# Kernel tuning notes

Hardware: AMD Instinct MI355X
Metric: run time of the kernel (lower is better)

Reference implementation:

```python
import jax, jax.numpy as jnp
import numpy as np

N = 50000; F = 128; H = 128; E = 800000; G = 512; C = 1000; CE = 64; L = 128
EPS = 1e-5

def gcn_conv(x, src, dst, W, b, num_nodes):
    # PyG GCNConv: add self loops, sym-normalize, aggregate at dst
    loop = jnp.arange(num_nodes)
    s = jnp.concatenate([src, loop])
    d = jnp.concatenate([dst, loop])
    deg = jax.ops.segment_sum(jnp.ones_like(d, dtype=x.dtype), d, num_segments=num_nodes)
    dinv = jnp.where(deg > 0, jax.lax.rsqrt(deg), 0.0)
    norm = dinv[s] * dinv[d]                      # [E+N]
    h = x @ W                                     # [N,H]
    msg = h[s] * norm[:, None]                    # gather + scale
    return jax.ops.segment_sum(msg, d, num_segments=num_nodes) + b

def layer_norm(x, w, b):
    mu = jnp.mean(x, axis=-1, keepdims=True)
    var = jnp.var(x, axis=-1, keepdims=True)
    return (x - mu) * jax.lax.rsqrt(var + EPS) * w + b

def setup_inputs() -> dict:
    key = jax.random.key(0)
    ks = jax.random.split(key, 16)
    x = jax.random.normal(ks[0], (N, F), dtype=jnp.float32)
    edge_index = jax.random.randint(ks[1], (2, E), 0, N)
    batch = jnp.sort(jax.random.randint(ks[2], (N,), 0, G))
    cell_lines = jax.random.randint(ks[3], (G,), 0, C)
    def kai(k, shape):
        fan_in = shape[0]
        bound = np.sqrt(6.0 / fan_in)
        return jax.random.uniform(k, shape, jnp.float32, -bound, bound)
    return {
        'x': x, 'edge_index': edge_index, 'batch': batch, 'cell_lines': cell_lines,
        'W1': kai(ks[4], (F, H)), 'b1': jnp.zeros((H,), jnp.float32),
        'W2': kai(ks[5], (H, H)), 'b2': jnp.zeros((H,), jnp.float32),
        'emb': jax.random.normal(ks[6], (C, CE), dtype=jnp.float32),
        'Wc': kai(ks[7], (H + CE, H)), 'bc': jnp.zeros((H,), jnp.float32),
        'lnc_w': jnp.ones((H,), jnp.float32), 'lnc_b': jnp.zeros((H,), jnp.float32),
        'Wf1': kai(ks[8], (H, H)), 'bf1': jnp.zeros((H,), jnp.float32),
        'ln1_w': jnp.ones((H,), jnp.float32), 'ln1_b': jnp.zeros((H,), jnp.float32),
        'Wf2': kai(ks[9], (H, L)), 'bf2': jnp.zeros((L,), jnp.float32),
    }

def reference(x, edge_index, batch, cell_lines, W1, b1, W2, b2, emb, Wc, bc,
              lnc_w, lnc_b, Wf1, bf1, ln1_w, ln1_b, Wf2, bf2):
    src, dst = edge_index[0], edge_index[1]
    h = jax.nn.relu(gcn_conv(x, src, dst, W1, b1, N))
    h = jax.nn.relu(gcn_conv(h, src, dst, W2, b2, N))
    g = jax.ops.segment_sum(h, batch, num_segments=G)          # global_add_pool [G,H]
    ce = emb[cell_lines]                                       # [G,CE]
    comb = jnp.concatenate([g, ce], axis=1)
    comb = jax.nn.relu(layer_norm(comb @ Wc + bc, lnc_w, lnc_b))
    out = jax.nn.relu(comb @ Wf1 + bf1)                        # dropout = identity (eval)
    out = layer_norm(out, ln1_w, ln1_b)
    return out @ Wf2 + bf2
```

## Files before the change

### kernel.cpp

```cpp
#include <hip/hip_runtime.h>

#define N_NODES 50000
#define NFEAT 128
#define NEDGE 800000
#define NGRAPH 512
#define NCE 64
#define EPS 1e-5f
#define NBUCK 196
#define EPB 4096
#define BCAP 6144

typedef short s8v __attribute__((ext_vector_type(8)));
typedef float f4v __attribute__((ext_vector_type(4)));

static __device__ __forceinline__ unsigned short f2bf(float f) {
    unsigned int u = __float_as_uint(f);
    unsigned int r = u + 0x7fffu + ((u >> 16) & 1u);
    return (unsigned short)(r >> 16);
}
static __device__ __forceinline__ float bf_lo(unsigned int packed) {
    return __uint_as_float(packed << 16);
}
static __device__ __forceinline__ float bf_hi(unsigned int packed) {
    return __uint_as_float(packed & 0xffff0000u);
}
static __device__ __forceinline__ float bf_us(unsigned short us) {
    return __uint_as_float(((unsigned int)us) << 16);
}

__global__ __launch_bounds__(256) void wcast_kernel(
    const float* __restrict__ W1, const float* __restrict__ W2,
    unsigned short* __restrict__ WT1, unsigned short* __restrict__ WT2,
    int* __restrict__ bucketCursor)
{
    if (blockIdx.x == 0 && blockIdx.y == 0 && threadIdx.x < NBUCK)
        bucketCursor[threadIdx.x] = 0;
    const float* W = blockIdx.y ? W2 : W1;
    unsigned short* WT = blockIdx.y ? WT2 : WT1;
    int idx = blockIdx.x * 256 + threadIdx.x;
    int k = idx >> 7, n = idx & 127;
    WT[n * 128 + k] = f2bf(W[idx]);
}

__global__ __launch_bounds__(256) void bucket_scatter_kernel(
    const int* __restrict__ ei, int* __restrict__ bucketCursor,
    unsigned int* __restrict__ recbuf, int E)
{
    __shared__ int hist[NBUCK];
    __shared__ int lbase[NBUCK];
    __shared__ int gbase[NBUCK];
    __shared__ int cur[NBUCK];
    __shared__ int scanbuf[256];
    __shared__ unsigned int staging[EPB];
    int tid = threadIdx.x;
    if (tid < NBUCK) { hist[tid] = 0; cur[tid] = 0; }
    __syncthreads();

    unsigned int rec[EPB / 256];
    int e0 = blockIdx.x * EPB + tid;
#pragma unroll
    for (int i = 0; i < EPB / 256; ++i) {
        int e = e0 + i * 256;
        if (e < E) {
            unsigned int sv = (unsigned)ei[e];
            unsigned int dv = (unsigned)ei[E + e];
            rec[i] = sv | (dv << 16);
            atomicAdd(&hist[dv >> 8], 1);
        } else {
            rec[i] = 0xffffffffu;
        }
    }
    __syncthreads();
    int v = (tid < NBUCK) ? hist[tid] : 0;
    scanbuf[tid] = v; __syncthreads();
    for (int off = 1; off < 256; off <<= 1) {
        int t = (tid >= off) ? scanbuf[tid - off] : 0;
        __syncthreads();
        scanbuf[tid] += t;
        __syncthreads();
    }
    if (tid < NBUCK) lbase[tid] = scanbuf[tid] - v;
    int total = scanbuf[255];
    if (tid < NBUCK) gbase[tid] = (v > 0) ? atomicAdd(&bucketCursor[tid], v) : 0;
    __syncthreads();
#pragma unroll
    for (int i = 0; i < EPB / 256; ++i) {
        if (rec[i] != 0xffffffffu) {
            int b = rec[i] >> 24;
            int loc = atomicAdd(&cur[b], 1);
            staging[lbase[b] + loc] = rec[i];
        }
    }
    __syncthreads();
    for (int s = tid; s < total; s += 256) {
        unsigned int r = staging[s];
        int b = r >> 24;
        int pos = gbase[b] + (s - lbase[b]);
        if (pos < BCAP) recbuf[(size_t)b * BCAP + pos] = r;
    }
}

__global__ __launch_bounds__(256) void bucket_csr_kernel(
    const unsigned int* __restrict__ recbuf, const int* __restrict__ bucketCursor,
    int* __restrict__ rowbeg, unsigned short* __restrict__ deg,
    float* __restrict__ dinv, unsigned short* __restrict__ colidx)
{
    __shared__ int cnt[256];
    __shared__ int cur[256];
    __shared__ int scanbuf[256];
    __shared__ unsigned short stage[BCAP];
    int b = blockIdx.x, tid = threadIdx.x;
    int base = b * BCAP;
    int len = bucketCursor[b]; if (len > BCAP) len = BCAP;
    cnt[tid] = 0;
    __syncthreads();
    for (int s = tid; s < len; s += 256) {
        unsigned int r = recbuf[base + s];
        atomicAdd(&cnt[(r >> 16) & 255], 1);
    }
    __syncthreads();
    int v = cnt[tid];
    scanbuf[tid] = v; __syncthreads();
    for (int off = 1; off < 256; off <<= 1) {
        int t = (tid >= off) ? scanbuf[tid - off] : 0;
        __syncthreads();
        scanbuf[tid] += t;
        __syncthreads();
    }
    int excl = scanbuf[tid] - v;
    int node = b * 256 + tid;
    if (node < N_NODES) {
        rowbeg[node] = base + excl;
        deg[node] = (unsigned short)v;
        dinv[node] = rsqrtf((float)v + 1.0f);
    }
    cur[tid] = excl;
    __syncthreads();
    for (int s = tid; s < len; s += 256) {
        unsigned int r = recbuf[base + s];
        int pos = atomicAdd(&cur[(r >> 16) & 255], 1);
        stage[pos] = (unsigned short)(r & 0xffffu);
    }
    __syncthreads();
    for (int s = tid; s < len; s += 256) colidx[base + s] = stage[s];
}

template<bool FP32IN>
__global__ __launch_bounds__(256) void gemm_mfma_kernel(
    const void* __restrict__ Ain, const unsigned short* __restrict__ WTg,
    const float* __restrict__ dinv, unsigned short* __restrict__ HS, int nrows)
{
    __shared__ unsigned short as[128 * 128];
    __shared__ unsigned short wt[128 * 128];
    const int tid = threadIdx.x;
    const int row0 = blockIdx.x * 128;

    {
        const uint4* src = reinterpret_cast<const uint4*>(WTg);
        uint4* dst = reinterpret_cast<uint4*>(wt);
#pragma unroll
        for (int i = 0; i < 8; ++i) dst[tid + i * 256] = src[tid + i * 256];
    }
    if (FP32IN) {
        const float* X = (const float*)Ain;
#pragma unroll
        for (int i = 0; i < 16; ++i) {
            int f = tid + i * 256;
            int r = f >> 5, c4 = f & 31;
            int rr = row0 + r; if (rr >= nrows) rr = nrows - 1;
            float4 v = *reinterpret_cast<const float4*>(&X[rr * 128 + c4 * 4]);
            ushort4 o;
            o.x = f2bf(v.x); o.y = f2bf(v.y); o.z = f2bf(v.z); o.w = f2bf(v.w);
            *reinterpret_cast<ushort4*>(&as[r * 128 + c4 * 4]) = o;
        }
    } else {
        const unsigned short* X = (const unsigned short*)Ain;
#pragma unroll
        for (int i = 0; i < 8; ++i) {
            int f = tid + i * 256;
            int r = f >> 4, c8 = f & 15;
            int rr = row0 + r; if (rr >= nrows) rr = nrows - 1;
            *reinterpret_cast<uint4*>(&as[r * 128 + c8 * 8]) =
                *reinterpret_cast<const uint4*>(&X[rr * 128 + c8 * 8]);
        }
    }
    __syncthreads();

    const int w = tid >> 6;
    const int lane = tid & 63;
    const int quad = lane >> 4;
    const int col0 = lane & 15;

    s8v afr[2][4];
#pragma unroll
    for (int rt = 0; rt < 2; ++rt)
#pragma unroll
        for (int kt = 0; kt < 4; ++kt)
            afr[rt][kt] = *reinterpret_cast<const s8v*>(
                &as[(w * 32 + rt * 16 + col0) * 128 + kt * 32 + quad * 8]);

    f4v acc[2][8];
#pragma unroll
    for (int rt = 0; rt < 2; ++rt)
#pragma unroll
        for (int nt = 0; nt < 8; ++nt)
            acc[rt][nt] = (f4v){0.f, 0.f, 0.f, 0.f};

#pragma unroll
    for (int nt = 0; nt < 8; ++nt) {
        s8v bfr[4];
#pragma unroll
        for (int kt = 0; kt < 4; ++kt)
            bfr[kt] = *reinterpret_cast<const s8v*>(
                &wt[(nt * 16 + col0) * 128 + kt * 32 + quad * 8]);
#pragma unroll
        for (int rt = 0; rt < 2; ++rt)
#pragma unroll
            for (int kt = 0; kt < 4; ++kt)
                acc[rt][nt] = __builtin_amdgcn_mfma_f32_16x16x32_bf16(
                    afr[rt][kt], bfr[kt], acc[rt][nt], 0, 0, 0);
    }

    float dv[2][4];
#pragma unroll
    for (int rt = 0; rt < 2; ++rt)
#pragma unroll
        for (int reg = 0; reg < 4; ++reg) {
            int r = row0 + w * 32 + rt * 16 + quad * 4 + reg;
            dv[rt][reg] = (r < nrows) ? dinv[r] : 0.f;
        }

#pragma unroll
    for (int rt = 0; rt < 2; ++rt)
#pragma unroll
        for (int nt = 0; nt < 8; ++nt)
#pragma unroll
            for (int reg = 0; reg < 4; ++reg) {
                int rl = w * 32 + rt * 16 + quad * 4 + reg;
                as[rl * 128 + nt * 16 + col0] = f2bf(acc[rt][nt][reg] * dv[rt][reg]);
            }
    __syncthreads();
#pragma unroll
    for (int i = 0; i < 8; ++i) {
        int f = tid + i * 256;
        int r = f >> 4, c8 = f & 15;
        if (row0 + r < nrows)
            *reinterpret_cast<uint4*>(&HS[(size_t)(row0 + r) * 128 + c8 * 8]) =
                *reinterpret_cast<const uint4*>(&as[r * 128 + c8 * 8]);
    }
}

__global__ __launch_bounds__(256) void aggregate_kernel(
    const uint2* __restrict__ H2,
    const int* __restrict__ rowbeg, const unsigned short* __restrict__ deg,
    const unsigned short* __restrict__ colidx,
    const float* __restrict__ dinv, const float* __restrict__ bias,
    uint2* __restrict__ OUT, int n)
{
    int wid = (blockIdx.x * blockDim.x + threadIdx.x) >> 6;
    int lane = threadIdx.x & 63;
    if (wid >= n) return;
    const int half = lane >> 5;
    const int sub = lane & 31;
    int beg = rowbeg[wid];
    int cnt = (int)deg[wid] + 1;
    float s0 = 0.f, s1 = 0.f, s2 = 0.f, s3 = 0.f;
    float r0 = 0.f, r1 = 0.f, r2 = 0.f, r3 = 0.f;
    for (int base = 0; base < cnt; base += 64) {
        int m = cnt - base; if (m > 64) m = 64;
        int p = base + lane;
        int idx = 0;
        if (lane < m) idx = (p == 0) ? wid : (int)colidx[beg + p - 1];
        int j = 0;
        for (; j + 16 <= m; j += 16) {
            uint2 t[8];
#pragma unroll
            for (int q = 0; q < 8; ++q) {
                int u = __shfl(idx, j + q * 2 + half);
                t[q] = H2[(size_t)u * 32 + sub];
            }
#pragma unroll
            for (int q = 0; q < 8; q += 2) {
                s0 += bf_lo(t[q].x); s1 += bf_hi(t[q].x);
                s2 += bf_lo(t[q].y); s3 += bf_hi(t[q].y);
                r0 += bf_lo(t[q + 1].x); r1 += bf_hi(t[q + 1].x);
                r2 += bf_lo(t[q + 1].y); r3 += bf_hi(t[q + 1].y);
            }
        }
        for (; j + 4 <= m; j += 4) {
            int ua = __shfl(idx, j + half);
            int ub = __shfl(idx, j + 2 + half);
            uint2 ta = H2[(size_t)ua * 32 + sub];
            uint2 tb = H2[(size_t)ub * 32 + sub];
            s0 += bf_lo(ta.x); s1 += bf_hi(ta.x);
            s2 += bf_lo(ta.y); s3 += bf_hi(ta.y);
            r0 += bf_lo(tb.x); r1 += bf_hi(tb.x);
            r2 += bf_lo(tb.y); r3 += bf_hi(tb.y);
        }
        if (j + 2 <= m) {
            int u = __shfl(idx, j + half);
            uint2 t = H2[(size_t)u * 32 + sub];
            s0 += bf_lo(t.x); s1 += bf_hi(t.x);
            s2 += bf_lo(t.y); s3 += bf_hi(t.y);
            j += 2;
        }
        if (j < m) {
            int u = __shfl(idx, j);
            uint2 t; t.x = 0u; t.y = 0u;
            if (half == 0) t = H2[(size_t)u * 32 + sub];
            s0 += bf_lo(t.x); s1 += bf_hi(t.x);
            s2 += bf_lo(t.y); s3 += bf_hi(t.y);
        }
    }
    s0 += r0; s1 += r1; s2 += r2; s3 += r3;
    s0 += __shfl_xor(s0, 32);
    s1 += __shfl_xor(s1, 32);
    s2 += __shfl_xor(s2, 32);
    s3 += __shfl_xor(s3, 32);
    if (half == 0) {
        float sc = dinv[wid];
        float4 bv = *reinterpret_cast<const float4*>(&bias[sub * 4]);
        float o0 = fmaxf(fmaf(s0, sc, bv.x), 0.f);
        float o1 = fmaxf(fmaf(s1, sc, bv.y), 0.f);
        float o2 = fmaxf(fmaf(s2, sc, bv.z), 0.f);
        float o3 = fmaxf(fmaf(s3, sc, bv.w), 0.f);
        uint2 o;
        o.x = (unsigned int)f2bf(o0) | ((unsigned int)f2bf(o1) << 16);
        o.y = (unsigned int)f2bf(o2) | ((unsigned int)f2bf(o3) << 16);
        OUT[(size_t)wid * 32 + sub] = o;
    }
}

__global__ __launch_bounds__(256) void tail_kernel(
    const unsigned short* __restrict__ h2b, const int* __restrict__ batch,
    const int* __restrict__ cell, const float* __restrict__ emb,
    const float* __restrict__ Wc, const float* __restrict__ bc,
    const float* __restrict__ lncw, const float* __restrict__ lncb,
    const float* __restrict__ Wf1, const float* __restrict__ bf1,
    const float* __restrict__ ln1w, const float* __restrict__ ln1b,
    const float* __restrict__ Wf2, const float* __restrict__ bf2,
    float* __restrict__ out)
{
    __shared__ __align__(16) float comb[192];
    __shared__ __align__(16) float part[8][132];
    __shared__ float red[4];
    __shared__ __align__(16) float vec[128];
    const int gi = blockIdx.x;
    const int tid = threadIdx.x;
    const int cg = tid & 31;
    const int ks = tid >> 5;

    int lo = 0, hi = N_NODES;
    while (lo < hi) { int mid = (lo + hi) >> 1; if (batch[mid] < gi) lo = mid + 1; else hi = mid; }
    int lo2 = lo, hi2 = N_NODES;
    while (lo2 < hi2) { int mid = (lo2 + hi2) >> 1; if (batch[mid] < gi + 1) lo2 = mid + 1; else hi2 = mid; }

    {
        int half = tid >> 7;
        int j = tid & 127;
        float acc = 0.f;
        for (int v = lo + half; v < lo2; v += 2)
            acc += bf_us(h2b[(size_t)v * 128 + j]);
        part[half][j] = acc;
    }
    __syncthreads();
    if (tid < 128) comb[tid] = part[0][tid] + part[1][tid];
    else if (tid < 192) comb[tid] = emb[cell[gi] * 64 + (tid - 128)];
    __syncthreads();

    {
        float c[24];
#pragma unroll
        for (int i = 0; i < 6; ++i) {
            float4 t = *reinterpret_cast<const float4*>(&comb[ks * 24 + i * 4]);
            c[i * 4 + 0] = t.x; c[i * 4 + 1] = t.y; c[i * 4 + 2] = t.z; c[i * 4 + 3] = t.w;
        }
        float a0 = 0.f, a1 = 0.f, a2 = 0.f, a3 = 0.f;
#pragma unroll
        for (int i = 0; i < 24; ++i) {
            const float4 w = *reinterpret_cast<const float4*>(&Wc[(ks * 24 + i) * 128 + cg * 4]);
            a0 = fmaf(c[i], w.x, a0);
            a1 = fmaf(c[i], w.y, a1);
            a2 = fmaf(c[i], w.z, a2);
            a3 = fmaf(c[i], w.w, a3);
        }
        float4 o; o.x = a0; o.y = a1; o.z = a2; o.w = a3;
        *reinterpret_cast<float4*>(&part[ks][cg * 4]) = o;
    }
    __syncthreads();
    {
        float y = 0.f;
        if (tid < 128) {
            y = bc[tid];
#pragma unroll
            for (int s = 0; s < 8; ++s) y += part[s][tid];
        }
        float s1 = (tid < 128) ? y : 0.f;
        float s2 = (tid < 128) ? y * y : 0.f;
        if (tid < 128) {
#pragma unroll
            for (int off = 32; off > 0; off >>= 1) {
                s1 += __shfl_down(s1, off);
                s2 += __shfl_down(s2, off);
            }
            if ((tid & 63) == 0) { red[(tid >> 6) * 2] = s1; red[(tid >> 6) * 2 + 1] = s2; }
        }
        __syncthreads();
        float mu = (red[0] + red[2]) * (1.f / 128.f);
        float ms = (red[1] + red[3]) * (1.f / 128.f);
        float var = ms - mu * mu;
        if (tid < 128) {
            float yv = (y - mu) * rsqrtf(var + EPS) * lncw[tid] + lncb[tid];
            vec[tid] = fmaxf(yv, 0.f);
        }
    }
    __syncthreads();

    {
        float c[16];
#pragma unroll
        for (int i = 0; i < 4; ++i) {
            float4 t = *reinterpret_cast<const float4*>(&vec[ks * 16 + i * 4]);
            c[i * 4 + 0] = t.x; c[i * 4 + 1] = t.y; c[i * 4 + 2] = t.z; c[i * 4 + 3] = t.w;
        }
        float a0 = 0.f, a1 = 0.f, a2 = 0.f, a3 = 0.f;
#pragma unroll
        for (int i = 0; i < 16; ++i) {
            const float4 w = *reinterpret_cast<const float4*>(&Wf1[(ks * 16 + i) * 128 + cg * 4]);
            a0 = fmaf(c[i], w.x, a0);
            a1 = fmaf(c[i], w.y, a1);
            a2 = fmaf(c[i], w.z, a2);
            a3 = fmaf(c[i], w.w, a3);
        }
        float4 o; o.x = a0; o.y = a1; o.z = a2; o.w = a3;
        *reinterpret_cast<float4*>(&part[ks][cg * 4]) = o;
    }
    __syncthreads();
    {
        float y = 0.f;
        if (tid < 128) {
            y = bf1[tid];
#pragma unroll
            for (int s = 0; s < 8; ++s) y += part[s][tid];
            y = fmaxf(y, 0.f);
        }
        float s1 = (tid < 128) ? y : 0.f;
        float s2 = (tid < 128) ? y * y : 0.f;
        if (tid < 128) {
#pragma unroll
            for (int off = 32; off > 0; off >>= 1) {
                s1 += __shfl_down(s1, off);
                s2 += __shfl_down(s2, off);
            }
            if ((tid & 63) == 0) { red[(tid >> 6) * 2] = s1; red[(tid >> 6) * 2 + 1] = s2; }
        }
        __syncthreads();
        float mu = (red[0] + red[2]) * (1.f / 128.f);
        float ms = (red[1] + red[3]) * (1.f / 128.f);
        float var = ms - mu * mu;
        if (tid < 128)
            vec[tid] = (y - mu) * rsqrtf(var + EPS) * ln1w[tid] + ln1b[tid];
    }
    __syncthreads();

    {
        float c[16];
#pragma unroll
        for (int i = 0; i < 4; ++i) {
            float4 t = *reinterpret_cast<const float4*>(&vec[ks * 16 + i * 4]);
            c[i * 4 + 0] = t.x; c[i * 4 + 1] = t.y; c[i * 4 + 2] = t.z; c[i * 4 + 3] = t.w;
        }
        float a0 = 0.f, a1 = 0.f, a2 = 0.f, a3 = 0.f;
#pragma unroll
        for (int i = 0; i < 16; ++i) {
            const float4 w = *reinterpret_cast<const float4*>(&Wf2[(ks * 16 + i) * 128 + cg * 4]);
            a0 = fmaf(c[i], w.x, a0);
            a1 = fmaf(c[i], w.y, a1);
            a2 = fmaf(c[i], w.z, a2);
            a3 = fmaf(c[i], w.w, a3);
        }
        float4 o; o.x = a0; o.y = a1; o.z = a2; o.w = a3;
        *reinterpret_cast<float4*>(&part[ks][cg * 4]) = o;
    }
    __syncthreads();
    if (tid < 128) {
        float y = bf2[tid];
#pragma unroll
        for (int s = 0; s < 8; ++s) y += part[s][tid];
        out[gi * 128 + tid] = y;
    }
}

extern "C" void kernel_launch(void* const* d_in, const int* in_sizes, int n_in,
                              void* d_out, int out_size, void* d_ws, size_t ws_size,
                              hipStream_t stream) {
    const float* x    = (const float*)d_in[0];
    const int*   ei   = (const int*)d_in[1];
    const int*   batch= (const int*)d_in[2];
    const int*   cell = (const int*)d_in[3];
    const float* W1   = (const float*)d_in[4];
    const float* b1   = (const float*)d_in[5];
    const float* W2   = (const float*)d_in[6];
    const float* b2   = (const float*)d_in[7];
    const float* emb  = (const float*)d_in[8];
    const float* Wc   = (const float*)d_in[9];
    const float* bc   = (const float*)d_in[10];
    const float* lncw = (const float*)d_in[11];
    const float* lncb = (const float*)d_in[12];
    const float* Wf1  = (const float*)d_in[13];
    const float* bf1  = (const float*)d_in[14];
    const float* ln1w = (const float*)d_in[15];
    const float* ln1b = (const float*)d_in[16];
    const float* Wf2  = (const float*)d_in[17];
    const float* bf2  = (const float*)d_in[18];
    float* out = (float*)d_out;

    char* ws = (char*)d_ws;
    size_t off = 0;
    auto alloc = [&](size_t bytes) { char* p = ws + off; off = (off + bytes + 255) & ~size_t(255); return p; };
    float*          dinv        = (float*)alloc(N_NODES * 4);
    int*            rowbeg      = (int*)  alloc(N_NODES * 4);
    unsigned short* deg         = (unsigned short*)alloc(N_NODES * 2);
    unsigned short* colidx      = (unsigned short*)alloc((size_t)NBUCK * BCAP * 2);
    int*            bucketCursor= (int*)  alloc(NBUCK * 4);
    unsigned int*   recbuf      = (unsigned int*)alloc((size_t)NBUCK * BCAP * 4);
    unsigned short* wt1         = (unsigned short*)alloc(128 * 128 * 2);
    unsigned short* wt2         = (unsigned short*)alloc(128 * 128 * 2);
    unsigned short* hs          = (unsigned short*)alloc((size_t)N_NODES * 128 * 2);
    unsigned short* h1          = (unsigned short*)alloc((size_t)N_NODES * 128 * 2);
    unsigned short* h2b         = (unsigned short*)alloc((size_t)N_NODES * 128 * 2);

    const int nbEdge = (NEDGE + EPB - 1) / EPB;
    const int nbGemm = (N_NODES + 127) / 128;
    const int nbAgg  = (N_NODES + 3) / 4;

    wcast_kernel<<<dim3(64, 2), 256, 0, stream>>>(W1, W2, wt1, wt2, bucketCursor);

    bucket_scatter_kernel<<<nbEdge, 256, 0, stream>>>(ei, bucketCursor, recbuf, NEDGE);
    bucket_csr_kernel<<<NBUCK, 256, 0, stream>>>(recbuf, bucketCursor, rowbeg, deg, dinv, colidx);

    gemm_mfma_kernel<true><<<nbGemm, 256, 0, stream>>>(x, wt1, dinv, hs, N_NODES);
    aggregate_kernel<<<nbAgg, 256, 0, stream>>>((const uint2*)hs, rowbeg, deg, colidx,
                                                dinv, b1, (uint2*)h1, N_NODES);
    gemm_mfma_kernel<false><<<nbGemm, 256, 0, stream>>>(h1, wt2, dinv, hs, N_NODES);
    aggregate_kernel<<<nbAgg, 256, 0, stream>>>((const uint2*)hs, rowbeg, deg, colidx,
                                                dinv, b2, (uint2*)h2b, N_NODES);
    tail_kernel<<<NGRAPH, 256, 0, stream>>>(h2b, batch, cell, emb, Wc, bc, lncw, lncb,
                                            Wf1, bf1, ln1w, ln1b, Wf2, bf2, out);
}
```

Baseline: 243.2 us.

## Use per-block fixed bucket slots, fuse weight cast, widen aggregate loads

Bucket scatter now writes each block's records into a fixed per-(bucket, block) slot of 64 entries and records per-slot counts. This removes the global atomic cursor and its zeroing, which lets the weight-cast work fold into the same launch and drops one kernel. The CSR kernel walks those slots using the counts. The aggregation kernel switches from 8-byte to 16-byte row loads, with four rows per wavefront step instead of two. The trade-offs are a much larger, sparsely filled record buffer that the CSR kernel must scan, and edges beyond 64 per slot are silently dropped.

```diff
diff --git a/kernel.cpp b/kernel.cpp
--- a/kernel.cpp
+++ b/kernel.cpp
@@ -8,6 +8,8 @@
 #define EPS 1e-5f
 #define NBUCK 196
 #define EPB 4096
+#define NSCAT 196
+#define CPB 64
 #define BCAP 6144
 
 typedef short s8v __attribute__((ext_vector_type(8)));
@@ -28,36 +30,33 @@
     return __uint_as_float(((unsigned int)us) << 16);
 }
 
-__global__ __launch_bounds__(256) void wcast_kernel(
+__global__ __launch_bounds__(256) void scatter_wcast_kernel(
+    const int* __restrict__ ei,
     const float* __restrict__ W1, const float* __restrict__ W2,
     unsigned short* __restrict__ WT1, unsigned short* __restrict__ WT2,
-    int* __restrict__ bucketCursor)
+    unsigned int* __restrict__ recbuf, unsigned short* __restrict__ cnts, int E)
 {
-    if (blockIdx.x == 0 && blockIdx.y == 0 && threadIdx.x < NBUCK)
-        bucketCursor[threadIdx.x] = 0;
-    const float* W = blockIdx.y ? W2 : W1;
-    unsigned short* WT = blockIdx.y ? WT2 : WT1;
-    int idx = blockIdx.x * 256 + threadIdx.x;
-    int k = idx >> 7, n = idx & 127;
-    WT[n * 128 + k] = f2bf(W[idx]);
-}
-
-__global__ __launch_bounds__(256) void bucket_scatter_kernel(
-    const int* __restrict__ ei, int* __restrict__ bucketCursor,
-    unsigned int* __restrict__ recbuf, int E)
-{
+    int bid = blockIdx.x;
+    int tid = threadIdx.x;
+    if (bid >= NSCAT) {
+        int wb = bid - NSCAT;
+        const float* W = (wb & 1) ? W2 : W1;
+        unsigned short* WT = (wb & 1) ? WT2 : WT1;
+        int idx = (wb >> 1) * 256 + tid;
+        int k = idx >> 7, nn = idx & 127;
+        WT[nn * 128 + k] = f2bf(W[idx]);
+        return;
+    }
     __shared__ int hist[NBUCK];
     __shared__ int lbase[NBUCK];
-    __shared__ int gbase[NBUCK];
     __shared__ int cur[NBUCK];
     __shared__ int scanbuf[256];
     __shared__ unsigned int staging[EPB];
-    int tid = threadIdx.x;
     if (tid < NBUCK) { hist[tid] = 0; cur[tid] = 0; }
     __syncthreads();
 
     unsigned int rec[EPB / 256];
-    int e0 = blockIdx.x * EPB + tid;
+    int e0 = bid * EPB + tid;
 #pragma unroll
     for (int i = 0; i < EPB / 256; ++i) {
         int e = e0 + i * 256;
@@ -81,7 +80,6 @@
     }
     if (tid < NBUCK) lbase[tid] = scanbuf[tid] - v;
     int total = scanbuf[255];
-    if (tid < NBUCK) gbase[tid] = (v > 0) ? atomicAdd(&bucketCursor[tid], v) : 0;
     __syncthreads();
 #pragma unroll
     for (int i = 0; i < EPB / 256; ++i) {
@@ -92,16 +90,18 @@
         }
     }
     __syncthreads();
+    if (tid < NBUCK) cnts[bid * NBUCK + tid] = (unsigned short)min(v, CPB);
     for (int s = tid; s < total; s += 256) {
         unsigned int r = staging[s];
         int b = r >> 24;
-        int pos = gbase[b] + (s - lbase[b]);
-        if (pos < BCAP) recbuf[(size_t)b * BCAP + pos] = r;
+        int pos = s - lbase[b];
+        if (pos < CPB)
+            recbuf[((size_t)b * NSCAT + bid) * CPB + pos] = r;
     }
 }
 
 __global__ __launch_bounds__(256) void bucket_csr_kernel(
-    const unsigned int* __restrict__ recbuf, const int* __restrict__ bucketCursor,
+    const unsigned int* __restrict__ recbuf, const unsigned short* __restrict__ cnts,
     int* __restrict__ rowbeg, unsigned short* __restrict__ deg,
     float* __restrict__ dinv, unsigned short* __restrict__ colidx)
 {
@@ -110,13 +110,17 @@
     __shared__ int scanbuf[256];
     __shared__ unsigned short stage[BCAP];
     int b = blockIdx.x, tid = threadIdx.x;
-    int base = b * BCAP;
-    int len = bucketCursor[b]; if (len > BCAP) len = BCAP;
+    const unsigned int* rb = recbuf + (size_t)b * NSCAT * CPB;
     cnt[tid] = 0;
     __syncthreads();
-    for (int s = tid; s < len; s += 256) {
-        unsigned int r = recbuf[base + s];
-        atomicAdd(&cnt[(r >> 16) & 255], 1);
+    for (int s = tid; s < NSCAT * CPB; s += 256) {
+        int blk = s >> 6;
+        int pos = s & 63;
+        int c = (int)cnts[blk * NBUCK + b];
+        if (pos < c) {
+            unsigned int r = rb[s];
+            atomicAdd(&cnt[(r >> 16) & 255], 1);
+        }
     }
     __syncthreads();
     int v = cnt[tid];
@@ -128,21 +132,27 @@
         __syncthreads();
     }
     int excl = scanbuf[tid] - v;
+    int len = scanbuf[255];
     int node = b * 256 + tid;
     if (node < N_NODES) {
-        rowbeg[node] = base + excl;
+        rowbeg[node] = b * BCAP + excl;
         deg[node] = (unsigned short)v;
         dinv[node] = rsqrtf((float)v + 1.0f);
     }
     cur[tid] = excl;
     __syncthreads();
-    for (int s = tid; s < len; s += 256) {
-        unsigned int r = recbuf[base + s];
-        int pos = atomicAdd(&cur[(r >> 16) & 255], 1);
-        stage[pos] = (unsigned short)(r & 0xffffu);
-    }
-    __syncthreads();
-    for (int s = tid; s < len; s += 256) colidx[base + s] = stage[s];
+    for (int s = tid; s < NSCAT * CPB; s += 256) {
+        int blk = s >> 6;
+        int pos = s & 63;
+        int c = (int)cnts[blk * NBUCK + b];
+        if (pos < c) {
+            unsigned int r = rb[s];
+            int p = atomicAdd(&cur[(r >> 16) & 255], 1);
+            stage[p] = (unsigned short)(r & 0xffffu);
+        }
+    }
+    __syncthreads();
+    for (int s = tid; s < len; s += 256) colidx[b * BCAP + s] = stage[s];
 }
 
 template<bool FP32IN>
@@ -250,84 +260,88 @@
     }
 }
 
+static __device__ __forceinline__ void addrow(float* a, uint4 t) {
+    a[0] += bf_lo(t.x); a[1] += bf_hi(t.x);
+    a[2] += bf_lo(t.y); a[3] += bf_hi(t.y);
+    a[4] += bf_lo(t.z); a[5] += bf_hi(t.z);
+    a[6] += bf_lo(t.w); a[7] += bf_hi(t.w);
+}
 __global__ __launch_bounds__(256) void aggregate_kernel(
-    const uint2* __restrict__ H2,
+    const uint4* __restrict__ H4,
     const int* __restrict__ rowbeg, const unsigned short* __restrict__ deg,
     const unsigned short* __restrict__ colidx,
     const float* __restrict__ dinv, const float* __restrict__ bias,
-    uint2* __restrict__ OUT, int n)
+    uint4* __restrict__ OUT, int n)
 {
     int wid = (blockIdx.x * blockDim.x + threadIdx.x) >> 6;
     int lane = threadIdx.x & 63;
     if (wid >= n) return;
-    const int half = lane >> 5;
-    const int sub = lane & 31;
+    const int qd = lane >> 4;
+    const int sub = lane & 15;
     int beg = rowbeg[wid];
     int cnt = (int)deg[wid] + 1;
-    float s0 = 0.f, s1 = 0.f, s2 = 0.f, s3 = 0.f;
-    float r0 = 0.f, r1 = 0.f, r2 = 0.f, r3 = 0.f;
+    float accA[8] = {0.f, 0.f, 0.f, 0.f, 0.f, 0.f, 0.f, 0.f};
+    float accB[8] = {0.f, 0.f, 0.f, 0.f, 0.f, 0.f, 0.f, 0.f};
     for (int base = 0; base < cnt; base += 64) {
         int m = cnt - base; if (m > 64) m = 64;
         int p = base + lane;
         int idx = 0;
         if (lane < m) idx = (p == 0) ? wid : (int)colidx[beg + p - 1];
         int j = 0;
-        for (; j + 16 <= m; j += 16) {
-            uint2 t[8];
+        for (; j + 32 <= m; j += 32) {
+            uint4 t[8];
 #pragma unroll
             for (int q = 0; q < 8; ++q) {
-                int u = __shfl(idx, j + q * 2 + half);
-                t[q] = H2[(size_t)u * 32 + sub];
+                int u = __shfl(idx, j + q * 4 + qd);
+                t[q] = H4[(size_t)u * 16 + sub];
             }
 #pragma unroll
             for (int q = 0; q < 8; q += 2) {
-                s0 += bf_lo(t[q].x); s1 += bf_hi(t[q].x);
-                s2 += bf_lo(t[q].y); s3 += bf_hi(t[q].y);
-                r0 += bf_lo(t[q + 1].x); r1 += bf_hi(t[q + 1].x);
-                r2 += bf_lo(t[q + 1].y); r3 += bf_hi(t[q + 1].y);
+                addrow(accA, t[q]);
+                addrow(accB, t[q + 1]);
             }
         }
-        for (; j + 4 <= m; j += 4) {
-            int ua = __shfl(idx, j + half);
-            int ub = __shfl(idx, j + 2 + half);
-            uint2 ta = H2[(size_t)ua * 32 + sub];
-            uint2 tb = H2[(size_t)ub * 32 + sub];
-            s0 += bf_lo(ta.x); s1 += bf_hi(ta.x);
-            s2 += bf_lo(ta.y); s3 += bf_hi(ta.y);
-            r0 += bf_lo(tb.x); r1 += bf_hi(tb.x);
-            r2 += bf_lo(tb.y); r3 += bf_hi(tb.y);
-        }
-        if (j + 2 <= m) {
-            int u = __shfl(idx, j + half);
-            uint2 t = H2[(size_t)u * 32 + sub];
-            s0 += bf_lo(t.x); s1 += bf_hi(t.x);
-            s2 += bf_lo(t.y); s3 += bf_hi(t.y);
-            j += 2;
-        }
-        if (j < m) {
-            int u = __shfl(idx, j);
-            uint2 t; t.x = 0u; t.y = 0u;
-            if (half == 0) t = H2[(size_t)u * 32 + sub];
-            s0 += bf_lo(t.x); s1 += bf_hi(t.x);
-            s2 += bf_lo(t.y); s3 += bf_hi(t.y);
-        }
-    }
-    s0 += r0; s1 += r1; s2 += r2; s3 += r3;
-    s0 += __shfl_xor(s0, 32);
-    s1 += __shfl_xor(s1, 32);
-    s2 += __shfl_xor(s2, 32);
-    s3 += __shfl_xor(s3, 32);
-    if (half == 0) {
+        for (; j + 8 <= m; j += 8) {
+            int u0 = __shfl(idx, j + qd);
+            int u1 = __shfl(idx, j + 4 + qd);
+            uint4 t0 = H4[(size_t)u0 * 16 + sub];
+            uint4 t1 = H4[(size_t)u1 * 16 + sub];
+            addrow(accA, t0);
+            addrow(accB, t1);
+        }
+        for (; j < m; j += 4) {
+            int sl = j + qd;
+            int u = __shfl(idx, sl < m ? sl : m - 1);
+            uint4 t = H4[(size_t)u * 16 + sub];
+            if (sl >= m) { t.x = 0u; t.y = 0u; t.z = 0u; t.w = 0u; }
+            addrow(accA, t);
+        }
+    }
+#pragma unroll
+    for (int i = 0; i < 8; ++i) accA[i] += accB[i];
+#pragma unroll
+    for (int i = 0; i < 8; ++i) {
+        accA[i] += __shfl_xor(accA[i], 16);
+        accA[i] += __shfl_xor(accA[i], 32);
+    }
+    if (qd == 0) {
         float sc = dinv[wid];
-        float4 bv = *reinterpret_cast<const float4*>(&bias[sub * 4]);
-        float o0 = fmaxf(fmaf(s0, sc, bv.x), 0.f);
-        float o1 = fmaxf(fmaf(s1, sc, bv.y), 0.f);
-        float o2 = fmaxf(fmaf(s2, sc, bv.z), 0.f);
-        float o3 = fmaxf(fmaf(s3, sc, bv.w), 0.f);
-        uint2 o;
+        float4 bv0 = *reinterpret_cast<const float4*>(&bias[sub * 8]);
+        float4 bv1 = *reinterpret_cast<const float4*>(&bias[sub * 8 + 4]);
+        float o0 = fmaxf(fmaf(accA[0], sc, bv0.x), 0.f);
+        float o1 = fmaxf(fmaf(accA[1], sc, bv0.y), 0.f);
+        float o2 = fmaxf(fmaf(accA[2], sc, bv0.z), 0.f);
+        float o3 = fmaxf(fmaf(accA[3], sc, bv0.w), 0.f);
+        float o4 = fmaxf(fmaf(accA[4], sc, bv1.x), 0.f);
+        float o5 = fmaxf(fmaf(accA[5], sc, bv1.y), 0.f);
+        float o6 = fmaxf(fmaf(accA[6], sc, bv1.z), 0.f);
+        float o7 = fmaxf(fmaf(accA[7], sc, bv1.w), 0.f);
+        uint4 o;
         o.x = (unsigned int)f2bf(o0) | ((unsigned int)f2bf(o1) << 16);
         o.y = (unsigned int)f2bf(o2) | ((unsigned int)f2bf(o3) << 16);
-        OUT[(size_t)wid * 32 + sub] = o;
+        o.z = (unsigned int)f2bf(o4) | ((unsigned int)f2bf(o5) << 16);
+        o.w = (unsigned int)f2bf(o6) | ((unsigned int)f2bf(o7) << 16);
+        OUT[(size_t)wid * 16 + sub] = o;
     }
 }
 
@@ -518,33 +532,31 @@
     char* ws = (char*)d_ws;
     size_t off = 0;
     auto alloc = [&](size_t bytes) { char* p = ws + off; off = (off + bytes + 255) & ~size_t(255); return p; };
-    float*          dinv        = (float*)alloc(N_NODES * 4);
-    int*            rowbeg      = (int*)  alloc(N_NODES * 4);
-    unsigned short* deg         = (unsigned short*)alloc(N_NODES * 2);
-    unsigned short* colidx      = (unsigned short*)alloc((size_t)NBUCK * BCAP * 2);
-    int*            bucketCursor= (int*)  alloc(NBUCK * 4);
-    unsigned int*   recbuf      = (unsigned int*)alloc((size_t)NBUCK * BCAP * 4);
-    unsigned short* wt1         = (unsigned short*)alloc(128 * 128 * 2);
-    unsigned short* wt2         = (unsigned short*)alloc(128 * 128 * 2);
-    unsigned short* hs          = (unsigned short*)alloc((size_t)N_NODES * 128 * 2);
-    unsigned short* h1          = (unsigned short*)alloc((size_t)N_NODES * 128 * 2);
-    unsigned short* h2b         = (unsigned short*)alloc((size_t)N_NODES * 128 * 2);
-
-    const int nbEdge = (NEDGE + EPB - 1) / EPB;
+    float*          dinv   = (float*)alloc(N_NODES * 4);
+    int*            rowbeg = (int*)  alloc(N_NODES * 4);
+    unsigned short* deg    = (unsigned short*)alloc(N_NODES * 2);
+    unsigned short* colidx = (unsigned short*)alloc((size_t)NBUCK * BCAP * 2);
+    unsigned int*   recbuf = (unsigned int*)alloc((size_t)NBUCK * NSCAT * CPB * 4);
+    unsigned short* cnts   = (unsigned short*)alloc((size_t)NSCAT * NBUCK * 2);
+    unsigned short* wt1    = (unsigned short*)alloc(128 * 128 * 2);
+    unsigned short* wt2    = (unsigned short*)alloc(128 * 128 * 2);
+    unsigned short* hs     = (unsigned short*)alloc((size_t)N_NODES * 128 * 2);
+    unsigned short* h1     = (unsigned short*)alloc((size_t)N_NODES * 128 * 2);
+    unsigned short* h2b    = (unsigned short*)alloc((size_t)N_NODES * 128 * 2);
+
     const int nbGemm = (N_NODES + 127) / 128;
     const int nbAgg  = (N_NODES + 3) / 4;
 
-    wcast_kernel<<<dim3(64, 2), 256, 0, stream>>>(W1, W2, wt1, wt2, bucketCursor);
-
-    bucket_scatter_kernel<<<nbEdge, 256, 0, stream>>>(ei, bucketCursor, recbuf, NEDGE);
-    bucket_csr_kernel<<<NBUCK, 256, 0, stream>>>(recbuf, bucketCursor, rowbeg, deg, dinv, colidx);
+    scatter_wcast_kernel<<<NSCAT + 128, 256, 0, stream>>>(ei, W1, W2, wt1, wt2,
+                                                          recbuf, cnts, NEDGE);
+    bucket_csr_kernel<<<NBUCK, 256, 0, stream>>>(recbuf, cnts, rowbeg, deg, dinv, colidx);
 
     gemm_mfma_kernel<true><<<nbGemm, 256, 0, stream>>>(x, wt1, dinv, hs, N_NODES);
-    aggregate_kernel<<<nbAgg, 256, 0, stream>>>((const uint2*)hs, rowbeg, deg, colidx,
-                                                dinv, b1, (uint2*)h1, N_NODES);
+    aggregate_kernel<<<nbAgg, 256, 0, stream>>>((const uint4*)hs, rowbeg, deg, colidx,
+                                                dinv, b1, (uint4*)h1, N_NODES);
     gemm_mfma_kernel<false><<<nbGemm, 256, 0, stream>>>(h1, wt2, dinv, hs, N_NODES);
-    aggregate_kernel<<<nbAgg, 256, 0, stream>>>((const uint2*)hs, rowbeg, deg, colidx,
-                                                dinv, b2, (uint2*)h2b, N_NODES);
+    aggregate_kernel<<<nbAgg, 256, 0, stream>>>((const uint4*)hs, rowbeg, deg, colidx,
+                                                dinv, b2, (uint4*)h2b, N_NODES);
     tail_kernel<<<NGRAPH, 256, 0, stream>>>(h2b, batch, cell, emb, Wc, bc, lncw, lncb,
                                             Wf1, bf1, ln1w, ln1b, Wf2, bf2, out);
 }
```

Result: slower. 280.6 us (+15.4%).
